# Optimization experiments

Hardware: AMD Instinct MI355X
Metric: run time of the kernel (lower is better)

## Reference

```python
import jax, jax.numpy as jnp
import numpy as np

N = 100000       # nodes
E = 1600000      # edges (avg degree 16)
ND = 64          # node_dim
ED = 1           # edge_dim
HD = 128         # hidden_dim of message MLP


def setup_inputs() -> dict:
    key = jax.random.key(0)
    ks = jax.random.split(key, 12)
    x = jax.random.normal(ks[0], (N, ND), dtype=jnp.float32)
    edge_index = jax.random.randint(ks[1], (2, E), 0, N, dtype=jnp.int32)
    edge_attr = jax.random.normal(ks[2], (E, ED), dtype=jnp.float32)
    # message_net: Linear(2*ND+ED -> HD), ReLU, Linear(HD -> ND); torch default uniform init
    s1 = 1.0 / np.sqrt(2 * ND + ED)
    W1 = jax.random.uniform(ks[3], (HD, 2 * ND + ED), minval=-s1, maxval=s1, dtype=jnp.float32)
    b1 = jax.random.uniform(ks[4], (HD,), minval=-s1, maxval=s1, dtype=jnp.float32)
    s2 = 1.0 / np.sqrt(HD)
    W2 = jax.random.uniform(ks[5], (ND, HD), minval=-s2, maxval=s2, dtype=jnp.float32)
    b2 = jax.random.uniform(ks[6], (ND,), minval=-s2, maxval=s2, dtype=jnp.float32)
    # GRUCell(input=ND, hidden=ND): weight_ih [3*ND, ND], weight_hh [3*ND, ND]
    sg = 1.0 / np.sqrt(ND)
    W_ih = jax.random.uniform(ks[7], (3 * ND, ND), minval=-sg, maxval=sg, dtype=jnp.float32)
    b_ih = jax.random.uniform(ks[8], (3 * ND,), minval=-sg, maxval=sg, dtype=jnp.float32)
    W_hh = jax.random.uniform(ks[9], (3 * ND, ND), minval=-sg, maxval=sg, dtype=jnp.float32)
    b_hh = jax.random.uniform(ks[10], (3 * ND,), minval=-sg, maxval=sg, dtype=jnp.float32)
    return {"x": x, "edge_index": edge_index, "edge_attr": edge_attr,
            "W1": W1, "b1": b1, "W2": W2, "b2": b2,
            "W_ih": W_ih, "b_ih": b_ih, "W_hh": W_hh, "b_hh": b_hh}


def reference(x, edge_index, edge_attr, W1, b1, W2, b2, W_ih, b_ih, W_hh, b_hh):
    src, dst = edge_index[0], edge_index[1]
    # gather + concat + 2-layer MLP message  -> [E, ND]
    m = jnp.concatenate([x[src], x[dst], edge_attr], axis=-1)      # [E, 2*ND+ED]
    m = jax.nn.relu(m @ W1.T + b1) @ W2.T + b2                     # [E, ND]
    # scatter-add aggregate to destination nodes
    aggr = jnp.zeros_like(x).at[dst].add(m)                        # [N, ND]
    # torch GRUCell: input=aggr, hidden=x
    gi = aggr @ W_ih.T + b_ih                                      # [N, 3*ND]
    gh = x @ W_hh.T + b_hh                                         # [N, 3*ND]
    i_r, i_z, i_n = jnp.split(gi, 3, axis=-1)
    h_r, h_z, h_n = jnp.split(gh, 3, axis=-1)
    r = jax.nn.sigmoid(i_r + h_r)
    z = jax.nn.sigmoid(i_z + h_z)
    n = jnp.tanh(i_n + r * h_n)
    return (1.0 - z) * n + z * x
```

## Files before the change

kernel.cpp:

```cpp
#include <hip/hip_runtime.h>

#define NN 100000
#define NE 1600000
#define ND 64
#define HD 128
#define NPB 16
#define NBK (NN / NPB)
#define NCB 98
#define NBA 256
#define CHA 6250

typedef float f32x4 __attribute__((ext_vector_type(4)));
typedef short s16x8 __attribute__((ext_vector_type(8)));

static __device__ __forceinline__ short f2bf(float f) {
    union { float f; unsigned u; } v; v.f = f;
    unsigned r = (v.u + 0x7fffu + ((v.u >> 16) & 1u)) >> 16;
    return (short)r;
}

#define LSW(n, k)  (((n) << 7) + ((((k) >> 3) ^ ((n) & 15)) << 3) + ((k) & 7))
#define LSW64(n, k) (((n) << 6) + ((((k) >> 3) ^ ((n) & 7)) << 3) + ((k) & 7))

__global__ __launch_bounds__(256) void conv_bf16(const float* __restrict__ x,
                                                 short* __restrict__ xb) {
    const int NG = NN * ND / 8;
    for (int g = blockIdx.x * 256 + threadIdx.x; g < NG; g += gridDim.x * 256) {
        const float4 a = ((const float4*)x)[g * 2];
        const float4 b = ((const float4*)x)[g * 2 + 1];
        s16x8 o;
        o[0] = f2bf(a.x); o[1] = f2bf(a.y); o[2] = f2bf(a.z); o[3] = f2bf(a.w);
        o[4] = f2bf(b.x); o[5] = f2bf(b.y); o[6] = f2bf(b.z); o[7] = f2bf(b.w);
        ((s16x8*)xb)[g] = o;
    }
}

__global__ __launch_bounds__(1024) void histA(const int* __restrict__ ei,
                                              int* __restrict__ gHistA,
                                              int* __restrict__ histN) {
    __shared__ int h[NCB];
    const int tid = threadIdx.x;
    if (tid < NCB) h[tid] = 0;
    __syncthreads();
    const int base = blockIdx.x * CHA;
    for (int i = tid; i < CHA; i += 1024) {
        const int d = ei[NE + base + i];
        atomicAdd(&h[d >> 10], 1);
        atomicAdd(&histN[d], 1);
    }
    __syncthreads();
    if (tid < NCB) gHistA[tid * NBA + blockIdx.x] = h[tid];
}

__global__ __launch_bounds__(1024) void scanA(int* __restrict__ g,
                                              int* __restrict__ rowptrB,
                                              int* __restrict__ ticket) {
    __shared__ int A[1024], B[1024];
    const int t = threadIdx.x;
    const int M = NCB * NBA;
    int v[25];
    int s = 0;
    #pragma unroll
    for (int j = 0; j < 25; ++j) {
        const int i = t * 25 + j;
        v[j] = (i < M) ? g[i] : 0;
        s += v[j];
    }
    A[t] = s;
    __syncthreads();
    int* src = A; int* dst = B;
    for (int off = 1; off < 1024; off <<= 1) {
        int val = src[t];
        if (t >= off) val += src[t - off];
        dst[t] = val;
        __syncthreads();
        int* tmp = src; src = dst; dst = tmp;
    }
    int run = t ? src[t - 1] : 0;
    #pragma unroll
    for (int j = 0; j < 25; ++j) {
        const int i = t * 25 + j;
        if (i < M) { g[i] = run; run += v[j]; }
    }
    if (t == 0) { *ticket = 0; rowptrB[NBK] = NE; }
}

__global__ __launch_bounds__(1024) void scatterA(
    const int* __restrict__ ei, const float* __restrict__ ea,
    const int* __restrict__ gBaseA, int2* __restrict__ tsd,
    float* __restrict__ tea) {
    __shared__ int cur[NCB];
    const int tid = threadIdx.x;
    if (tid < NCB) cur[tid] = gBaseA[tid * NBA + blockIdx.x];
    __syncthreads();
    const int base = blockIdx.x * CHA;
    for (int i = tid; i < CHA; i += 1024) {
        const int e = base + i;
        const int sv = ei[e], d = ei[NE + e];
        const float av = ea[e];
        const int pos = atomicAdd(&cur[d >> 10], 1);
        tsd[pos] = make_int2(sv, d);
        tea[pos] = av;
    }
}

__global__ __launch_bounds__(1024) void scatterB(
    const int2* __restrict__ tsd, const float* __restrict__ tea,
    const int* __restrict__ histN, const int* __restrict__ gBaseA,
    int2* __restrict__ rsd, float* __restrict__ rea,
    int* __restrict__ rowptrB) {
    __shared__ int A[1024], B[1024];
    __shared__ int cur[1024];
    const int c = blockIdx.x;
    const int t = threadIdx.x;
    const int n = (c << 10) + t;
    const int cnt = (n < NN) ? histN[n] : 0;
    A[t] = cnt;
    __syncthreads();
    int* src = A; int* dst = B;
    for (int off = 1; off < 1024; off <<= 1) {
        int val = src[t];
        if (t >= off) val += src[t - off];
        dst[t] = val;
        __syncthreads();
        int* tmp = src; src = dst; dst = tmp;
    }
    const int off0  = t ? src[t - 1] : 0;
    const int base  = gBaseA[c * NBA];
    const int tend  = (c == NCB - 1) ? NE : gBaseA[(c + 1) * NBA];
    cur[t] = base + off0;
    if ((t & 15) == 0 && n < NN) rowptrB[n >> 4] = base + off0;
    __syncthreads();
    for (int i = base + t; i < tend; i += 1024) {
        const int2 sd = tsd[i];
        const float av = tea[i];
        const int pos = atomicAdd(&cur[sd.y - (c << 10)], 1);
        rsd[pos] = sd;
        rea[pos] = av;
    }
}

__global__ __launch_bounds__(512) void msg_mfma3(
    const short* __restrict__ xb, const int2* __restrict__ rsd,
    const float* __restrict__ rea, const int* __restrict__ rowptrB,
    int* __restrict__ ticket,
    const float* __restrict__ W1, const float* __restrict__ b1,
    const float* __restrict__ W2, const float* __restrict__ b2,
    float* __restrict__ aggr)
{
    __shared__ short w1lds[128 * 128];
    __shared__ short w2lds[64 * 128];
    __shared__ short vbuf[8 * 16 * 128];
    __shared__ float albuf[8 * NPB * 64];

    const int tid = threadIdx.x;
    for (int i = tid; i < 128 * 128; i += 512) {
        int n = i >> 7, k = i & 127;
        w1lds[LSW(n, k)] = f2bf(W1[n * 129 + k]);
    }
    for (int i = tid; i < 64 * 128; i += 512) {
        int n = i >> 7, k = i & 127;
        w2lds[LSW(n, k)] = f2bf(W2[n * 128 + k]);
    }
    __syncthreads();

    const int lane = tid & 63;
    const int w    = tid >> 6;
    const int nlo  = lane & 15;
    const int q    = lane >> 4;

    float w1l[8], b1v[8], b2v[4];
    #pragma unroll
    for (int t = 0; t < 8; ++t) {
        w1l[t] = W1[(nlo + 16 * t) * 129 + 128];
        b1v[t] = b1[nlo + 16 * t];
    }
    #pragma unroll
    for (int t = 0; t < 4; ++t) b2v[t] = b2[nlo + 16 * t];

    short* myv = vbuf + w * (16 * 128);
    float* vf  = (float*)myv;
    float* al  = albuf + w * (NPB * 64);

    for (;;) {
        int bk = 0;
        if (lane == 0) bk = atomicAdd(ticket, 1);
        bk = __shfl(bk, 0, 64);
        if (bk >= NBK) break;

        const int n0    = bk * NPB;
        const int start = rowptrB[bk];
        const int end   = rowptrB[bk + 1];

        const f32x4 z = {0.f, 0.f, 0.f, 0.f};
        #pragma unroll
        for (int j = 0; j < 4; ++j) ((f32x4*)al)[lane + 64 * j] = z;

        if (start < end) {
            int  idx0 = min(start + nlo, end - 1);
            int2 sd   = rsd[idx0];
            float eav = rea[idx0];
            s16x8 a0 = *(const s16x8*)(xb + sd.x * ND + (q << 3));
            s16x8 a1 = *(const s16x8*)(xb + sd.x * ND + 32 + (q << 3));
            s16x8 a2 = *(const s16x8*)(xb + sd.y * ND + (q << 3));
            s16x8 a3 = *(const s16x8*)(xb + sd.y * ND + 32 + (q << 3));

            for (int p = start; p < end; p += 16) {
                const int dv = sd.y;

                const int  idxn = min(p + 16 + nlo, end - 1);
                const int2 sdn  = rsd[idxn];
                const float ean = rea[idxn];

                f32x4 acc[8];
                #pragma unroll
                for (int t = 0; t < 8; ++t) { acc[t][0] = b1v[t]; acc[t][1] = b1v[t]; acc[t][2] = b1v[t]; acc[t][3] = b1v[t]; }

                __builtin_amdgcn_s_setprio(1);
                #pragma unroll
                for (int kk = 0; kk < 4; ++kk) {
                    const s16x8 af = (kk == 0) ? a0 : (kk == 1) ? a1 : (kk == 2) ? a2 : a3;
                    const int chunk = ((kk * 4 + q) ^ nlo) << 3;
                    #pragma unroll
                    for (int t = 0; t < 8; ++t) {
                        const s16x8 bf = *(const s16x8*)(w1lds + ((nlo + 16 * t) << 7) + chunk);
                        acc[t] = __builtin_amdgcn_mfma_f32_16x16x32_bf16(af, bf, acc[t], 0, 0, 0);
                    }
                }
                __builtin_amdgcn_s_setprio(0);

                const s16x8 n0_ = *(const s16x8*)(xb + sdn.x * ND + (q << 3));
                const s16x8 n1_ = *(const s16x8*)(xb + sdn.x * ND + 32 + (q << 3));
                const s16x8 n2_ = *(const s16x8*)(xb + sdn.y * ND + (q << 3));
                const s16x8 n3_ = *(const s16x8*)(xb + sdn.y * ND + 32 + (q << 3));

                float ear[4];
                #pragma unroll
                for (int r = 0; r < 4; ++r) ear[r] = __shfl(eav, q * 4 + r, 64);
                #pragma unroll
                for (int t = 0; t < 8; ++t) {
                    #pragma unroll
                    for (int r = 0; r < 4; ++r) {
                        const float hv = fmaxf(acc[t][r] + ear[r] * w1l[t], 0.f);
                        const int m = q * 4 + r;
                        const int k = nlo + 16 * t;
                        myv[LSW(m, k)] = f2bf(hv);
                    }
                }

                f32x4 acc2[4];
                #pragma unroll
                for (int t = 0; t < 4; ++t) { acc2[t][0] = b2v[t]; acc2[t][1] = b2v[t]; acc2[t][2] = b2v[t]; acc2[t][3] = b2v[t]; }

                __builtin_amdgcn_s_setprio(1);
                #pragma unroll
                for (int kk = 0; kk < 4; ++kk) {
                    const int chunk = ((kk * 4 + q) ^ nlo) << 3;
                    const s16x8 af = *(const s16x8*)(myv + (nlo << 7) + chunk);
                    #pragma unroll
                    for (int t = 0; t < 4; ++t) {
                        const s16x8 bf = *(const s16x8*)(w2lds + ((nlo + 16 * t) << 7) + chunk);
                        acc2[t] = __builtin_amdgcn_mfma_f32_16x16x32_bf16(af, bf, acc2[t], 0, 0, 0);
                    }
                }
                __builtin_amdgcn_s_setprio(0);

                #pragma unroll
                for (int t = 0; t < 4; ++t) {
                    #pragma unroll
                    for (int r = 0; r < 4; ++r) {
                        const int m = q * 4 + r;
                        vf[m * 64 + ((nlo + 16 * t) ^ (q << 3))] = acc2[t][r];
                    }
                }

                const int nrows = min(16, end - p);
                float vals[16];
                #pragma unroll
                for (int r = 0; r < 16; ++r)
                    vals[r] = vf[r * 64 + (lane ^ ((r >> 2) << 3))];

                int   prev = __builtin_amdgcn_readlane(dv, 0);
                float sum  = vals[0];
                #pragma unroll
                for (int r = 1; r < 16; ++r) {
                    if (r < nrows) {
                        const int dd = __builtin_amdgcn_readlane(dv, r);
                        if (dd == prev) sum += vals[r];
                        else {
                            al[(prev - n0) * 64 + lane] += sum;
                            prev = dd; sum = vals[r];
                        }
                    }
                }
                al[(prev - n0) * 64 + lane] += sum;

                sd = sdn; eav = ean;
                a0 = n0_; a1 = n1_; a2 = n2_; a3 = n3_;
            }
        }

        f32x4* dstv = (f32x4*)(aggr + n0 * 64);
        #pragma unroll
        for (int j = 0; j < 4; ++j)
            dstv[lane + 64 * j] = ((f32x4*)al)[lane + 64 * j];
    }
}

__global__ __launch_bounds__(512) void gru_mfma(
    const float* __restrict__ x, const float* __restrict__ aggr,
    const float* __restrict__ Wih, const float* __restrict__ bih,
    const float* __restrict__ Whh, const float* __restrict__ bhh,
    float* __restrict__ out)
{
    __shared__ short wi[192 * 64];
    __shared__ short wh[192 * 64];

    const int tid = threadIdx.x;
    for (int i = tid; i < 192 * 64; i += 512) {
        int n = i >> 6, k = i & 63;
        wi[LSW64(n, k)] = f2bf(Wih[n * 64 + k]);
        wh[LSW64(n, k)] = f2bf(Whh[n * 64 + k]);
    }
    __syncthreads();

    const int lane = tid & 63;
    const int w    = tid >> 6;
    const int nlo  = lane & 15;
    const int q    = lane >> 4;

    float bi[12], bh[12];
    #pragma unroll
    for (int t = 0; t < 12; ++t) { bi[t] = bih[16 * t + nlo]; bh[t] = bhh[16 * t + nlo]; }

    const int gw = blockIdx.x * 8 + w;
    const int nw = gridDim.x * 8;

    for (int tile = gw; tile < NN / 16; tile += nw) {
        const int n0 = tile * 16;
        f32x4 ai[12], ah[12];
        #pragma unroll
        for (int t = 0; t < 12; ++t) {
            ai[t][0] = bi[t]; ai[t][1] = bi[t]; ai[t][2] = bi[t]; ai[t][3] = bi[t];
            ah[t][0] = bh[t]; ah[t][1] = bh[t]; ah[t][2] = bh[t]; ah[t][3] = bh[t];
        }

        #pragma unroll
        for (int kk = 0; kk < 2; ++kk) {
            const int coff = (n0 + nlo) * ND + kk * 32 + q * 8;
            const float4 a0 = *(const float4*)(aggr + coff);
            const float4 a1 = *(const float4*)(aggr + coff + 4);
            const float4 x0 = *(const float4*)(x + coff);
            const float4 x1 = *(const float4*)(x + coff + 4);
            s16x8 fA, fX;
            fA[0] = f2bf(a0.x); fA[1] = f2bf(a0.y); fA[2] = f2bf(a0.z); fA[3] = f2bf(a0.w);
            fA[4] = f2bf(a1.x); fA[5] = f2bf(a1.y); fA[6] = f2bf(a1.z); fA[7] = f2bf(a1.w);
            fX[0] = f2bf(x0.x); fX[1] = f2bf(x0.y); fX[2] = f2bf(x0.z); fX[3] = f2bf(x0.w);
            fX[4] = f2bf(x1.x); fX[5] = f2bf(x1.y); fX[6] = f2bf(x1.z); fX[7] = f2bf(x1.w);
            const int chunk = kk * 4 + q;
            #pragma unroll
            for (int t = 0; t < 12; ++t) {
                const int rb = 16 * t + nlo;
                const int boff = (rb << 6) + (((chunk) ^ (rb & 7)) << 3);
                const s16x8 bI = *(const s16x8*)(wi + boff);
                const s16x8 bH = *(const s16x8*)(wh + boff);
                ai[t] = __builtin_amdgcn_mfma_f32_16x16x32_bf16(fA, bI, ai[t], 0, 0, 0);
                ah[t] = __builtin_amdgcn_mfma_f32_16x16x32_bf16(fX, bH, ah[t], 0, 0, 0);
            }
        }

        #pragma unroll
        for (int t = 0; t < 4; ++t) {
            #pragma unroll
            for (int r = 0; r < 4; ++r) {
                const int node = n0 + q * 4 + r;
                const int c    = nlo + 16 * t;
                const float rr = 1.f / (1.f + __expf(-(ai[t][r] + ah[t][r])));
                const float zz = 1.f / (1.f + __expf(-(ai[t + 4][r] + ah[t + 4][r])));
                const float nv = ai[t + 8][r] + rr * ah[t + 8][r];
                const float nn = 2.f / (1.f + __expf(-2.f * nv)) - 1.f;
                const float xv = x[node * ND + c];
                out[node * ND + c] = (1.f - zz) * nn + zz * xv;
            }
        }
    }
}

extern "C" void kernel_launch(void* const* d_in, const int* in_sizes, int n_in,
                              void* d_out, int out_size, void* d_ws, size_t ws_size,
                              hipStream_t stream) {
    const float* x   = (const float*)d_in[0];
    const int*   ei  = (const int*)d_in[1];
    const float* ea  = (const float*)d_in[2];
    const float* W1  = (const float*)d_in[3];
    const float* b1  = (const float*)d_in[4];
    const float* W2  = (const float*)d_in[5];
    const float* b2  = (const float*)d_in[6];
    const float* Wih = (const float*)d_in[7];
    const float* bih = (const float*)d_in[8];
    const float* Whh = (const float*)d_in[9];
    const float* bhh = (const float*)d_in[10];
    float* out = (float*)d_out;

    char* ws = (char*)d_ws;
    float* aggr    = (float*)(ws);
    int2*  tsd     = (int2*) (ws);
    float* tea     = (float*)(ws + 12800000);
    short* xb      = (short*)(ws + 25600000);
    int2*  rsd     = (int2*) (ws + 38400000);
    float* rea     = (float*)(ws + 51200000);
    int*   histN   = (int*)  (ws + 57600000);
    int*   gHistA  = (int*)  (ws + 58000000);
    int*   rowptrB = (int*)  (ws + 58100352);
    int*   ticket  = (int*)  (ws + 58125356);

    hipMemsetAsync(histN, 0, NN * sizeof(int), stream);

    hipLaunchKernelGGL(conv_bf16, dim3(512), dim3(256), 0, stream, x, xb);
    hipLaunchKernelGGL(histA, dim3(NBA), dim3(1024), 0, stream, ei, gHistA, histN);
    hipLaunchKernelGGL(scanA, dim3(1), dim3(1024), 0, stream,
                       gHistA, rowptrB, ticket);
    hipLaunchKernelGGL(scatterA, dim3(NBA), dim3(1024), 0, stream,
                       ei, ea, gHistA, tsd, tea);
    hipLaunchKernelGGL(scatterB, dim3(NCB), dim3(1024), 0, stream,
                       tsd, tea, histN, gHistA, rsd, rea, rowptrB);
    hipLaunchKernelGGL(msg_mfma3, dim3(256), dim3(512), 0, stream,
                       xb, rsd, rea, rowptrB, ticket, W1, b1, W2, b2, aggr);
    hipLaunchKernelGGL(gru_mfma, dim3(256), dim3(512), 0, stream,
                       x, aggr, Wih, bih, Whh, bhh, out);
}
```

Baseline: 551.1 us.

## Restructure two-pass edge sort: per-bucket local histograms, finer buckets, more message blocks

Drops the global per-node histogram (and its memset and global atomics) and instead has each coarse bucket block count its own nodes in shared memory from the partially sorted edges before scanning. Coarse buckets change from 1024 nodes by node>>10 to 400 nodes by division, with 250 bucket blocks and 64 histogram blocks. It also doubles the message kernel grid. This removes global atomic traffic on 1.6M edges, but scatterB now reads tsd twice and the first pass uses fewer blocks.

```diff
diff --git a/kernel.cpp b/kernel.cpp
--- a/kernel.cpp
+++ b/kernel.cpp
@@ -6,9 +6,12 @@
 #define HD 128
 #define NPB 16
 #define NBK (NN / NPB)
-#define NCB 98
-#define NBA 256
-#define CHA 6250
+#define NPCB 400
+#define NCB 250
+#define NBA 64
+#define CHA (NE / NBA)
+#define MSC (NCB * NBA)
+#define CSC 16
 
 typedef float f32x4 __attribute__((ext_vector_type(4)));
 typedef short s16x8 __attribute__((ext_vector_type(8)));
@@ -36,36 +39,26 @@
 }
 
 __global__ __launch_bounds__(1024) void histA(const int* __restrict__ ei,
-                                              int* __restrict__ gHistA,
-                                              int* __restrict__ histN) {
+                                              int* __restrict__ gHistA) {
     __shared__ int h[NCB];
     const int tid = threadIdx.x;
     if (tid < NCB) h[tid] = 0;
     __syncthreads();
     const int base = blockIdx.x * CHA;
-    for (int i = tid; i < CHA; i += 1024) {
-        const int d = ei[NE + base + i];
-        atomicAdd(&h[d >> 10], 1);
-        atomicAdd(&histN[d], 1);
-    }
+    for (int i = tid; i < CHA; i += 1024)
+        atomicAdd(&h[ei[NE + base + i] / NPCB], 1);
     __syncthreads();
     if (tid < NCB) gHistA[tid * NBA + blockIdx.x] = h[tid];
 }
 
 __global__ __launch_bounds__(1024) void scanA(int* __restrict__ g,
-                                              int* __restrict__ rowptrB,
                                               int* __restrict__ ticket) {
     __shared__ int A[1024], B[1024];
-    const int t = threadIdx.x;
-    const int M = NCB * NBA;
-    int v[25];
+    const int t  = threadIdx.x;
+    const int i0 = t * CSC;
+    const int i1 = min(i0 + CSC, MSC);
     int s = 0;
-    #pragma unroll
-    for (int j = 0; j < 25; ++j) {
-        const int i = t * 25 + j;
-        v[j] = (i < M) ? g[i] : 0;
-        s += v[j];
-    }
+    for (int i = i0; i < i1; ++i) s += g[i];
     A[t] = s;
     __syncthreads();
     int* src = A; int* dst = B;
@@ -77,12 +70,11 @@
         int* tmp = src; src = dst; dst = tmp;
     }
     int run = t ? src[t - 1] : 0;
-    #pragma unroll
-    for (int j = 0; j < 25; ++j) {
-        const int i = t * 25 + j;
-        if (i < M) { g[i] = run; run += v[j]; }
-    }
-    if (t == 0) { *ticket = 0; rowptrB[NBK] = NE; }
+    for (int i = i0; i < i1; ++i) {
+        const int v = g[i];
+        g[i] = run; run += v;
+    }
+    if (t == 0) *ticket = 0;
 }
 
 __global__ __launch_bounds__(1024) void scatterA(
@@ -98,7 +90,7 @@
         const int e = base + i;
         const int sv = ei[e], d = ei[NE + e];
         const float av = ea[e];
-        const int pos = atomicAdd(&cur[d >> 10], 1);
+        const int pos = atomicAdd(&cur[d / NPCB], 1);
         tsd[pos] = make_int2(sv, d);
         tea[pos] = av;
     }
@@ -106,35 +98,49 @@
 
 __global__ __launch_bounds__(1024) void scatterB(
     const int2* __restrict__ tsd, const float* __restrict__ tea,
-    const int* __restrict__ histN, const int* __restrict__ gBaseA,
+    const int* __restrict__ gBaseA,
     int2* __restrict__ rsd, float* __restrict__ rea,
     int* __restrict__ rowptrB) {
-    __shared__ int A[1024], B[1024];
-    __shared__ int cur[1024];
+    __shared__ int h[NPCB];
+    __shared__ int cur[NPCB];
+    __shared__ int A[512], B[512];
     const int c = blockIdx.x;
     const int t = threadIdx.x;
-    const int n = (c << 10) + t;
-    const int cnt = (n < NN) ? histN[n] : 0;
-    A[t] = cnt;
+    const int nb0  = c * NPCB;
+    const int base = gBaseA[c * NBA];
+    const int endc = (c + 1 < NCB) ? gBaseA[(c + 1) * NBA] : NE;
+
+    if (t < NPCB) h[t] = 0;
+    __syncthreads();
+    for (int i = base + t; i < endc; i += 1024)
+        atomicAdd(&h[tsd[i].y - nb0], 1);
+    __syncthreads();
+
+    if (t < 512) A[t] = (t < NPCB) ? h[t] : 0;
     __syncthreads();
     int* src = A; int* dst = B;
-    for (int off = 1; off < 1024; off <<= 1) {
-        int val = src[t];
-        if (t >= off) val += src[t - off];
-        dst[t] = val;
+    for (int off = 1; off < 512; off <<= 1) {
+        if (t < 512) {
+            int val = src[t];
+            if (t >= off) val += src[t - off];
+            dst[t] = val;
+        }
         __syncthreads();
         int* tmp = src; src = dst; dst = tmp;
     }
-    const int off0  = t ? src[t - 1] : 0;
-    const int base  = gBaseA[c * NBA];
-    const int tend  = (c == NCB - 1) ? NE : gBaseA[(c + 1) * NBA];
-    cur[t] = base + off0;
-    if ((t & 15) == 0 && n < NN) rowptrB[n >> 4] = base + off0;
-    __syncthreads();
-    for (int i = base + t; i < tend; i += 1024) {
+    if (t < NPCB) {
+        const int excl = t ? src[t - 1] : 0;
+        cur[t] = base + excl;
+        if ((t & (NPB - 1)) == 0)
+            rowptrB[(nb0 + t) >> 4] = base + excl;
+    }
+    if (c == NCB - 1 && t == 0) rowptrB[NBK] = NE;
+    __syncthreads();
+
+    for (int i = base + t; i < endc; i += 1024) {
         const int2 sd = tsd[i];
         const float av = tea[i];
-        const int pos = atomicAdd(&cur[sd.y - (c << 10)], 1);
+        const int pos = atomicAdd(&cur[sd.y - nb0], 1);
         rsd[pos] = sd;
         rea[pos] = av;
     }
@@ -409,22 +415,18 @@
     short* xb      = (short*)(ws + 25600000);
     int2*  rsd     = (int2*) (ws + 38400000);
     float* rea     = (float*)(ws + 51200000);
-    int*   histN   = (int*)  (ws + 57600000);
-    int*   gHistA  = (int*)  (ws + 58000000);
-    int*   rowptrB = (int*)  (ws + 58100352);
-    int*   ticket  = (int*)  (ws + 58125356);
-
-    hipMemsetAsync(histN, 0, NN * sizeof(int), stream);
+    int*   gHistA  = (int*)  (ws + 57600000);
+    int*   rowptrB = (int*)  (ws + 57664000);
+    int*   ticket  = (int*)  (ws + 57689004);
 
     hipLaunchKernelGGL(conv_bf16, dim3(512), dim3(256), 0, stream, x, xb);
-    hipLaunchKernelGGL(histA, dim3(NBA), dim3(1024), 0, stream, ei, gHistA, histN);
-    hipLaunchKernelGGL(scanA, dim3(1), dim3(1024), 0, stream,
-                       gHistA, rowptrB, ticket);
+    hipLaunchKernelGGL(histA, dim3(NBA), dim3(1024), 0, stream, ei, gHistA);
+    hipLaunchKernelGGL(scanA, dim3(1), dim3(1024), 0, stream, gHistA, ticket);
     hipLaunchKernelGGL(scatterA, dim3(NBA), dim3(1024), 0, stream,
                        ei, ea, gHistA, tsd, tea);
     hipLaunchKernelGGL(scatterB, dim3(NCB), dim3(1024), 0, stream,
-                       tsd, tea, histN, gHistA, rsd, rea, rowptrB);
-    hipLaunchKernelGGL(msg_mfma3, dim3(256), dim3(512), 0, stream,
+                       tsd, tea, gHistA, rsd, rea, rowptrB);
+    hipLaunchKernelGGL(msg_mfma3, dim3(512), dim3(512), 0, stream,
                        xb, rsd, rea, rowptrB, ticket, W1, b1, W2, b2, aggr);
     hipLaunchKernelGGL(gru_mfma, dim3(256), dim3(512), 0, stream,
                        x, aggr, Wih, bih, Whh, bhh, out);
```

After: 518.4 us, median of 3. 5.9% less time.
